# Kernel optimization log

Measured on AMD Instinct MI355X. Metric: run time of the kernel, lower is better.

Reference implementation:

```python
import jax, jax.numpy as jnp
import numpy as np

B, CQ, CKV, E = 8, 256, 256, 256
H, W = 64, 64
HP, WP = 32, 32


def setup_inputs() -> dict:
    key = jax.random.key(0)
    ks = jax.random.split(key, 6)
    C = jax.random.normal(ks[0], (B, CQ, H, W), dtype=jnp.float32)
    P = jax.random.normal(ks[1], (B, CKV, HP, WP), dtype=jnp.float32)
    # 1x1 conv weights, kaiming-ish scale; stored as [out_ch, in_ch]
    theta_w = jax.random.normal(ks[2], (E, CQ), dtype=jnp.float32) * (1.0 / np.sqrt(CQ))
    phi_w = jax.random.normal(ks[3], (E, CKV), dtype=jnp.float32) * (1.0 / np.sqrt(CKV))
    g_w = jax.random.normal(ks[4], (E, CKV), dtype=jnp.float32) * (1.0 / np.sqrt(CKV))
    out_w = jax.random.normal(ks[5], (CQ, E), dtype=jnp.float32) * (1.0 / np.sqrt(E))
    return {"C": C, "P": P, "theta_w": theta_w, "phi_w": phi_w, "g_w": g_w, "out_w": out_w}


def reference(C, P, theta_w, phi_w, g_w, out_w):
    b, _, h, w = C.shape
    e = theta_w.shape[0]
    # 1x1 convs are channel GEMMs
    theta_C = jnp.einsum('bchw,ec->behw', C, theta_w).reshape(b, e, h * w)   # [B,E,Nq]
    phi_P = jnp.einsum('bchw,ec->behw', P, phi_w).reshape(b, e, -1)          # [B,E,Nkv]
    g_P = jnp.einsum('bchw,ec->behw', P, g_w).reshape(b, e, -1)              # [B,E,Nkv]
    attn = jnp.einsum('ben,bem->bnm', theta_C, phi_P) / (e ** 0.5)           # [B,Nq,Nkv]
    attn = jax.nn.softmax(attn, axis=-1)
    out = jnp.einsum('bem,bnm->ben', g_P, attn).reshape(b, e, h, w)          # [B,E,H,W]
    out = jnp.einsum('behw,ce->bchw', out, out_w)                            # [B,CQ,H,W]
    return jnp.concatenate([C, out], axis=1)
```

## Files before the change

kernel.cpp:

```cpp
#include <hip/hip_runtime.h>


typedef __attribute__((ext_vector_type(8))) short short8;
typedef __attribute__((ext_vector_type(16))) float f32x16;
typedef unsigned short ushort_t;

__device__ __forceinline__ unsigned short f2bf(float f) {
    unsigned int u = __float_as_uint(f);
    u += 0x7FFFu + ((u >> 16) & 1u);
    return (unsigned short)(u >> 16);
}
__device__ __forceinline__ unsigned int pack2bf(float a, float b) {
    return (unsigned int)f2bf(a) | ((unsigned int)f2bf(b) << 16);
}
__device__ __forceinline__ void gload16(const ushort_t* g, ushort_t* l) {
    __builtin_amdgcn_global_load_lds(
        (const __attribute__((address_space(1))) unsigned int*)g,
        (__attribute__((address_space(3))) unsigned int*)l, 16, 0, 0);
}
__device__ __forceinline__ f32x16 zero16() {
    f32x16 z;
#pragma unroll
    for (int i = 0; i < 16; ++i) z[i] = 0.f;
    return z;
}

__global__ __launch_bounds__(256) void ct_cvt(const float* __restrict__ X,
                                              ushort_t* __restrict__ xT) {
    const int N = 4096;
    int b = blockIdx.z, c0 = blockIdx.y * 64, n0 = blockIdx.x * 64;
    int t = threadIdx.x;
    __shared__ float Xs[64][68];
    const float* Xb = X + ((size_t)b * 256 + c0) * N + n0;
    int cl = t >> 4, nl = (t & 15) * 4;
#pragma unroll
    for (int ci = 0; ci < 4; ++ci) {
        int c = ci * 16 + cl;
        float4 v = *(const float4*)(Xb + (size_t)c * N + nl);
        *(float4*)&Xs[c][nl] = v;
    }
    __syncthreads();
    ushort_t* xb = xT + (size_t)b * ((size_t)N * 256);
    int nl2 = t & 63, cgb = t >> 6;
#pragma unroll
    for (int cp = 0; cp < 2; ++cp) {
        int cg = cp * 4 + cgb;
        int cb = c0 + cg * 8;
        int n = n0 + nl2;
        short8 v;
#pragma unroll
        for (int u = 0; u < 8; ++u) v[u] = (short)f2bf(Xs[cg * 8 + u][nl2]);
        size_t i16 = ((size_t)(n >> 5) * 16 + (cb >> 4)) * 64 + ((cb >> 3) & 1) * 32 + (n & 31);
        *(short8*)(xb + i16 * 8) = v;
    }
}

__global__ __launch_bounds__(256) void prep_small(const float* __restrict__ P,
                                                  const float* __restrict__ thw,
                                                  const float* __restrict__ phw,
                                                  const float* __restrict__ ow,
                                                  const float* __restrict__ gw,
                                                  ushort_t* __restrict__ pT,
                                                  ushort_t* __restrict__ thc,
                                                  ushort_t* __restrict__ phc,
                                                  ushort_t* __restrict__ w2c) {
    int blk = blockIdx.x;
    int t = threadIdx.x;
    __shared__ float Xs[64][68];
    if (blk < 512) {
        const int N = 1024;
        int bx = blk & 15, by = (blk >> 4) & 3, b = blk >> 6;
        int n0 = bx * 64, c0 = by * 64;
        const float* Xb = P + ((size_t)b * 256 + c0) * N + n0;
        int cl = t >> 4, nl = (t & 15) * 4;
#pragma unroll
        for (int ci = 0; ci < 4; ++ci) {
            int c = ci * 16 + cl;
            *(float4*)&Xs[c][nl] = *(const float4*)(Xb + (size_t)c * N + nl);
        }
        __syncthreads();
        ushort_t* xb = pT + (size_t)b * ((size_t)N * 256);
        int nl2 = t & 63, cgb = t >> 6;
#pragma unroll
        for (int cp = 0; cp < 2; ++cp) {
            int cg = cp * 4 + cgb;
            int cb = c0 + cg * 8;
            int n = n0 + nl2;
            short8 v;
#pragma unroll
            for (int u = 0; u < 8; ++u) v[u] = (short)f2bf(Xs[cg * 8 + u][nl2]);
            size_t i16 = ((size_t)(n >> 5) * 16 + (cb >> 4)) * 64 + ((cb >> 3) & 1) * 32 + (n & 31);
            *(short8*)(xb + i16 * 8) = v;
        }
    } else if (blk < 1024) {
        int r = blk - 512;
        int which = r >> 8;
        int e = r & 255, c = t;
        const float* src = which ? phw : thw;
        ushort_t* dst = which ? phc : thc;
        int idx = ((((e >> 5) * 16 + (c >> 4)) * 64 + ((c >> 3) & 1) * 32 + (e & 31)) << 3) + (c & 7);
        dst[idx] = f2bf(src[e * 256 + c]);
    } else {
        int c0 = (blk - 1024) * 8;
        float acc[8] = {};
        for (int e = 0; e < 256; ++e) {
            float g = gw[e * 256 + t];
#pragma unroll
            for (int i = 0; i < 8; ++i) acc[i] += ow[(c0 + i) * 256 + e] * g;
        }
#pragma unroll
        for (int i = 0; i < 8; ++i) {
            int c = c0 + i, k = t;
            int idx = ((((c >> 5) * 16 + (k >> 4)) * 64 + ((k >> 3) & 1) * 32 + (c & 31)) << 3) + (k & 7);
            w2c[idx] = f2bf(acc[i]);
        }
    }
}

__global__ __launch_bounds__(256, 2) void proj_mfma(const ushort_t* __restrict__ thc,
                                                    const ushort_t* __restrict__ phc,
                                                    const ushort_t* __restrict__ w2c,
                                                    const ushort_t* __restrict__ cT,
                                                    const ushort_t* __restrict__ pT,
                                                    ushort_t* __restrict__ thetaA,
                                                    ushort_t* __restrict__ phiA,
                                                    ushort_t* __restrict__ gVx) {
    int blk = blockIdx.x;
    int tid = threadIdx.x, lane = tid & 63, wid = tid >> 6;
    int l31 = lane & 31, lh = lane >> 5;
    int role, b, nt;
    const ushort_t *Wc, *xTb;
    ushort_t* outp;
    float scale = 1.f;
    if (blk < 256) {
        role = 0; b = blk & 7; nt = blk >> 3;
        Wc = thc; xTb = cT + (size_t)b * 1048576; outp = thetaA + (size_t)b * 1048576;
        scale = 1.4426950408889634f / 16.0f;
    } else if (blk < 320) {
        int r = blk - 256; role = 1; b = r & 7; nt = r >> 3;
        Wc = phc; xTb = pT + (size_t)b * 262144; outp = phiA + (size_t)b * 262144;
    } else {
        int r = blk - 320; role = 2; b = r & 7; nt = r >> 3;
        Wc = w2c; xTb = pT + (size_t)b * 262144; outp = gVx + (size_t)b * 262144;
    }
    const int n0 = nt * 128 + wid * 32;
    const int ncr = (n0 >> 5) * 16;

    f32x16 o[8];
#pragma unroll
    for (int f = 0; f < 8; ++f) o[f] = zero16();

#pragma unroll
    for (int ks = 0; ks < 16; ++ks) {
        short8 xf = *(const short8*)(xTb + ((size_t)(ncr + ks) * 64 + lane) * 8);
#pragma unroll
        for (int f = 0; f < 8; ++f) {
            short8 wf = *(const short8*)(Wc + ((size_t)(f * 16 + ks) * 64 + lane) * 8);
            o[f] = __builtin_amdgcn_mfma_f32_32x32x16_bf16(wf, xf, o[f], 0, 0, 0);
        }
    }

    if (role < 2) {
#pragma unroll
        for (int f = 0; f < 8; ++f) {
#pragma unroll
            for (int rq = 0; rq < 4; ++rq) {
                uint2 st;
                st.x = pack2bf(o[f][4 * rq + 0] * scale, o[f][4 * rq + 1] * scale);
                st.y = pack2bf(o[f][4 * rq + 2] * scale, o[f][4 * rq + 3] * scale);
                size_t addr = ((size_t)(ncr + f * 2 + (rq >> 1)) * 64 + l31 + 32 * (rq & 1)) * 8 + 4 * lh;
                *(uint2*)(outp + addr) = st;
            }
        }
    } else {
        int kvq = (n0 >> 4) + (l31 >> 4);
        int lhw = 32 * ((l31 >> 3) & 1);
        int kl = l31 & 7;
#pragma unroll
        for (int f = 0; f < 8; ++f) {
#pragma unroll
            for (int r = 0; r < 16; ++r) {
                int crow = (r & 3) + 8 * (r >> 2) + 4 * lh;
                size_t addr = ((size_t)(f * 64 + kvq) * 64 + crow + lhw) * 8 + kl;
                outp[addr] = f2bf(o[f][r]);
            }
        }
    }
}

__global__ __launch_bounds__(512, 2) void attn7(const ushort_t* __restrict__ thetaA,
                                                const ushort_t* __restrict__ phiA,
                                                const ushort_t* __restrict__ gVx,
                                                const float* __restrict__ Cf,
                                                float* __restrict__ out) {
    const int b = blockIdx.x & 7, qt = blockIdx.x >> 3;
    const int tid = threadIdx.x, lane = tid & 63, wid = tid >> 6;
    const int l31 = lane & 31, lh = lane >> 5;
    const int h = wid >> 2, qg = wid & 3;

    __shared__ __align__(16) ushort_t smem[65536];
    __shared__ float rlS[4][32];

    const ushort_t* thA = thetaA + (size_t)b * 1048576;
    const ushort_t* phA = phiA + (size_t)b * 262144;
    const ushort_t* gVb = gVx + (size_t)b * 262144;

    auto stageK = [&](int j) {
        if ((wid & 2) == 0) {
            int hh = wid >> 2;
            const ushort_t* src = phA + (size_t)(2 * j + hh) * 8192 + (wid & 1) * 4096 + lane * 8;
            ushort_t* dst = smem + hh * 16384 + (j & 1) * 8192 + (wid & 1) * 4096;
#pragma unroll
            for (int i = 0; i < 8; ++i) gload16(src + i * 512, dst + i * 512);
        }
    };
    auto stageV = [&](int j) {
        if ((wid & 2) == 2) {
            int hh = wid >> 2;
#pragma unroll
            for (int cg2 = 0; cg2 < 4; ++cg2) {
                int cg = (wid & 1) * 4 + cg2;
#pragma unroll
                for (int jj = 0; jj < 2; ++jj) {
                    const ushort_t* src =
                        gVb + ((size_t)(cg * 64 + 4 * j + 2 * hh + jj) * 64 + lane) * 8;
                    ushort_t* dst = smem + 32768 + hh * 16384 + (j & 1) * 8192 + cg * 1024 + jj * 512;
                    gload16(src, dst);
                }
            }
        }
    };

    stageK(0); stageK(1); stageV(0);

    short8 qf[16];
    {
        const int qcr = (qt * 4 + qg) * 16;
#pragma unroll
        for (int ks = 0; ks < 16; ++ks)
            qf[ks] = *(const short8*)(thA + ((size_t)(qcr + ks) * 64 + lane) * 8);
    }

    f32x16 o[8];
#pragma unroll
    for (int f = 0; f < 8; ++f) o[f] = zero16();
    float rl = 0.f;

    const size_t cbase = (size_t)b * 1048576 + (size_t)qt * 128 + (size_t)l31 * 4;
    const size_t dofs = (size_t)b * 1048576;
    size_t cpo = 0;
    float4 cpv;

    asm volatile("s_waitcnt vmcnt(0)" ::: "memory");
    __builtin_amdgcn_s_barrier();
    __builtin_amdgcn_sched_barrier(0);

    f32x16 s = zero16();
    {
        const ushort_t* Kb = smem + h * 16384;
#pragma unroll
        for (int ks = 0; ks < 16; ++ks) {
            short8 kf = *(const short8*)(Kb + (size_t)ks * 512 + lane * 8);
            s = __builtin_amdgcn_mfma_f32_32x32x16_bf16(kf, qf[ks], s, 0, 0, 0);
        }
    }

    for (int it = 0; it < 16; ++it) {
        asm volatile("s_waitcnt vmcnt(0)" ::: "memory");
        __builtin_amdgcn_s_barrier();
        __builtin_amdgcn_sched_barrier(0);
        if (it < 14) stageK(it + 2);
        if (it < 15) stageV(it + 1);

        if (it > 0) *(float4*)(out + cpo + dofs) = cpv;
        cpo = cbase + (size_t)(it * 16 + 2 * wid + lh) * 4096;
        cpv = *(const float4*)(Cf + cpo);

        float ps = 0.f;
#pragma unroll
        for (int r = 0; r < 16; ++r) {
            s[r] = __builtin_amdgcn_exp2f(s[r]);
            ps += s[r];
        }
        ps += __shfl_xor(ps, 32);
        rl += ps;

        unsigned int a0 = pack2bf(s[0], s[1]),   b0 = pack2bf(s[4], s[5]);
        unsigned int a1 = pack2bf(s[2], s[3]),   b1 = pack2bf(s[6], s[7]);
        unsigned int a2 = pack2bf(s[8], s[9]),   b2 = pack2bf(s[12], s[13]);
        unsigned int a3 = pack2bf(s[10], s[11]), b3 = pack2bf(s[14], s[15]);
        asm volatile("v_permlane32_swap_b32 %0, %1" : "+v"(a0), "+v"(b0));
        asm volatile("v_permlane32_swap_b32 %0, %1" : "+v"(a1), "+v"(b1));
        asm volatile("v_permlane32_swap_b32 %0, %1" : "+v"(a2), "+v"(b2));
        asm volatile("v_permlane32_swap_b32 %0, %1" : "+v"(a3), "+v"(b3));
        union PW { unsigned int u[4]; short8 v; };
        PW p0; p0.u[0] = a0; p0.u[1] = a1; p0.u[2] = b0; p0.u[3] = b1;
        PW p1; p1.u[0] = a2; p1.u[1] = a3; p1.u[2] = b2; p1.u[3] = b3;

        const ushort_t* Vb = smem + 32768 + h * 16384 + (it & 1) * 8192;
        const ushort_t* Kb = smem + h * 16384 + ((it + 1) & 1) * 8192;
        __builtin_amdgcn_s_setprio(1);
        if (it < 15) {
            f32x16 sn = zero16();
#pragma unroll
            for (int ks2 = 0; ks2 < 2; ++ks2) {
                short8 pf = ks2 ? p1.v : p0.v;
#pragma unroll
                for (int f = 0; f < 8; ++f) {
                    short8 vf = *(const short8*)(Vb + (size_t)f * 1024 + ks2 * 512 + lane * 8);
                    o[f] = __builtin_amdgcn_mfma_f32_32x32x16_bf16(vf, pf, o[f], 0, 0, 0);
                    int ks = ks2 * 8 + f;
                    short8 kf = *(const short8*)(Kb + (size_t)ks * 512 + lane * 8);
                    sn = __builtin_amdgcn_mfma_f32_32x32x16_bf16(kf, qf[ks], sn, 0, 0, 0);
                }
            }
            s = sn;
        } else {
#pragma unroll
            for (int ks2 = 0; ks2 < 2; ++ks2) {
                short8 pf = ks2 ? p1.v : p0.v;
#pragma unroll
                for (int f = 0; f < 8; ++f) {
                    short8 vf = *(const short8*)(Vb + (size_t)f * 1024 + ks2 * 512 + lane * 8);
                    o[f] = __builtin_amdgcn_mfma_f32_32x32x16_bf16(vf, pf, o[f], 0, 0, 0);
                }
            }
        }
        __builtin_amdgcn_s_setprio(0);
        __builtin_amdgcn_sched_barrier(0);
    }

    *(float4*)(out + cpo + dofs) = cpv;

    __syncthreads();

    if (wid >= 4) {
        float* part = (float*)smem + (size_t)(wid - 4) * 8192;
#pragma unroll
        for (int f = 0; f < 8; ++f)
#pragma unroll
            for (int r = 0; r < 16; ++r) {
                int e = f * 32 + (r & 3) + 8 * (r >> 2) + 4 * lh;
                part[e * 32 + l31] = o[f][r];
            }
        if (lane < 32) rlS[wid - 4][l31] = rl;
    }
    __syncthreads();
    if (wid < 4) {
        float inv = 1.f / (rl + rlS[wid][l31]);
        const float* part = (const float*)smem + (size_t)wid * 8192;
        float* ob = out + (size_t)b * 2097152 + (size_t)256 * 4096 + qt * 128 + qg * 32 + l31;
#pragma unroll
        for (int f = 0; f < 8; ++f)
#pragma unroll
            for (int r = 0; r < 16; ++r) {
                int e = f * 32 + (r & 3) + 8 * (r >> 2) + 4 * lh;
                ob[(size_t)e * 4096] = (o[f][r] + part[e * 32 + l31]) * inv;
            }
    }
}


extern "C" void kernel_launch(void* const* d_in, const int* in_sizes, int n_in,
                              void* d_out, int out_size, void* d_ws, size_t ws_size,
                              hipStream_t stream) {
    const float* C       = (const float*)d_in[0];
    const float* P       = (const float*)d_in[1];
    const float* theta_w = (const float*)d_in[2];
    const float* phi_w   = (const float*)d_in[3];
    const float* g_w     = (const float*)d_in[4];
    const float* out_w   = (const float*)d_in[5];
    float* out = (float*)d_out;

    ushort_t* ws = (ushort_t*)d_ws;
    ushort_t* thetaA = ws;
    ushort_t* cT     = ws + 8388608;
    ushort_t* phiA   = ws + 16777216;
    ushort_t* pT     = ws + 18874368;
    ushort_t* gVx    = ws + 20971520;
    ushort_t* thWc   = ws + 23068672;
    ushort_t* phWc   = ws + 23134208;
    ushort_t* w2c    = ws + 23199744;

    prep_small<<<1056, 256, 0, stream>>>(P, theta_w, phi_w, out_w, g_w,
                                         pT, thWc, phWc, w2c);
    ct_cvt<<<dim3(64, 4, 8), 256, 0, stream>>>(C, cT);
    proj_mfma<<<384, 256, 0, stream>>>(thWc, phWc, w2c, cT, pT, thetaA, phiA, gVx);
    attn7<<<256, 512, 0, stream>>>(thetaA, phiA, gVx, C, out);
}
```

Measured before the change: 119.6 us.

## Fuse theta projection and C passthrough copy into attention kernel

Removes the separate C transpose/convert kernel and the theta projection blocks. The attention kernel now loads its 128-query tile of C into shared memory, writes the passthrough half of the output, and computes the scaled theta projection with MFMA directly into Q fragments using permlane swaps. This avoids writing and re-reading the bf16 cT and thetaA intermediates and drops one launch. In exchange, the attention kernel does extra work up front, uses more shared memory, and no longer overlaps the C copy with its main loop.

```diff
diff --git a/kernel.cpp b/kernel.cpp
--- a/kernel.cpp
+++ b/kernel.cpp
@@ -23,36 +23,6 @@
 #pragma unroll
     for (int i = 0; i < 16; ++i) z[i] = 0.f;
     return z;
-}
-
-__global__ __launch_bounds__(256) void ct_cvt(const float* __restrict__ X,
-                                              ushort_t* __restrict__ xT) {
-    const int N = 4096;
-    int b = blockIdx.z, c0 = blockIdx.y * 64, n0 = blockIdx.x * 64;
-    int t = threadIdx.x;
-    __shared__ float Xs[64][68];
-    const float* Xb = X + ((size_t)b * 256 + c0) * N + n0;
-    int cl = t >> 4, nl = (t & 15) * 4;
-#pragma unroll
-    for (int ci = 0; ci < 4; ++ci) {
-        int c = ci * 16 + cl;
-        float4 v = *(const float4*)(Xb + (size_t)c * N + nl);
-        *(float4*)&Xs[c][nl] = v;
-    }
-    __syncthreads();
-    ushort_t* xb = xT + (size_t)b * ((size_t)N * 256);
-    int nl2 = t & 63, cgb = t >> 6;
-#pragma unroll
-    for (int cp = 0; cp < 2; ++cp) {
-        int cg = cp * 4 + cgb;
-        int cb = c0 + cg * 8;
-        int n = n0 + nl2;
-        short8 v;
-#pragma unroll
-        for (int u = 0; u < 8; ++u) v[u] = (short)f2bf(Xs[cg * 8 + u][nl2]);
-        size_t i16 = ((size_t)(n >> 5) * 16 + (cb >> 4)) * 64 + ((cb >> 3) & 1) * 32 + (n & 31);
-        *(short8*)(xb + i16 * 8) = v;
-    }
 }
 
 __global__ __launch_bounds__(256) void prep_small(const float* __restrict__ P,
@@ -117,32 +87,19 @@
     }
 }
 
-__global__ __launch_bounds__(256, 2) void proj_mfma(const ushort_t* __restrict__ thc,
-                                                    const ushort_t* __restrict__ phc,
+__global__ __launch_bounds__(256, 2) void proj_mfma(const ushort_t* __restrict__ phc,
                                                     const ushort_t* __restrict__ w2c,
-                                                    const ushort_t* __restrict__ cT,
                                                     const ushort_t* __restrict__ pT,
-                                                    ushort_t* __restrict__ thetaA,
                                                     ushort_t* __restrict__ phiA,
                                                     ushort_t* __restrict__ gVx) {
     int blk = blockIdx.x;
     int tid = threadIdx.x, lane = tid & 63, wid = tid >> 6;
     int l31 = lane & 31, lh = lane >> 5;
-    int role, b, nt;
-    const ushort_t *Wc, *xTb;
-    ushort_t* outp;
-    float scale = 1.f;
-    if (blk < 256) {
-        role = 0; b = blk & 7; nt = blk >> 3;
-        Wc = thc; xTb = cT + (size_t)b * 1048576; outp = thetaA + (size_t)b * 1048576;
-        scale = 1.4426950408889634f / 16.0f;
-    } else if (blk < 320) {
-        int r = blk - 256; role = 1; b = r & 7; nt = r >> 3;
-        Wc = phc; xTb = pT + (size_t)b * 262144; outp = phiA + (size_t)b * 262144;
-    } else {
-        int r = blk - 320; role = 2; b = r & 7; nt = r >> 3;
-        Wc = w2c; xTb = pT + (size_t)b * 262144; outp = gVx + (size_t)b * 262144;
-    }
+    int role = blk >> 6;
+    int r = blk & 63, b = r & 7, nt = r >> 3;
+    const ushort_t* Wc = role ? w2c : phc;
+    const ushort_t* xTb = pT + (size_t)b * 262144;
+    ushort_t* outp = (role ? gVx : phiA) + (size_t)b * 262144;
     const int n0 = nt * 128 + wid * 32;
     const int ncr = (n0 >> 5) * 16;
 
@@ -160,14 +117,14 @@
         }
     }
 
-    if (role < 2) {
+    if (!role) {
 #pragma unroll
         for (int f = 0; f < 8; ++f) {
 #pragma unroll
             for (int rq = 0; rq < 4; ++rq) {
                 uint2 st;
-                st.x = pack2bf(o[f][4 * rq + 0] * scale, o[f][4 * rq + 1] * scale);
-                st.y = pack2bf(o[f][4 * rq + 2] * scale, o[f][4 * rq + 3] * scale);
+                st.x = pack2bf(o[f][4 * rq + 0], o[f][4 * rq + 1]);
+                st.y = pack2bf(o[f][4 * rq + 2], o[f][4 * rq + 3]);
                 size_t addr = ((size_t)(ncr + f * 2 + (rq >> 1)) * 64 + l31 + 32 * (rq & 1)) * 8 + 4 * lh;
                 *(uint2*)(outp + addr) = st;
             }
@@ -179,16 +136,16 @@
 #pragma unroll
         for (int f = 0; f < 8; ++f) {
 #pragma unroll
-            for (int r = 0; r < 16; ++r) {
-                int crow = (r & 3) + 8 * (r >> 2) + 4 * lh;
+            for (int r2 = 0; r2 < 16; ++r2) {
+                int crow = (r2 & 3) + 8 * (r2 >> 2) + 4 * lh;
                 size_t addr = ((size_t)(f * 64 + kvq) * 64 + crow + lhw) * 8 + kl;
-                outp[addr] = f2bf(o[f][r]);
-            }
-        }
-    }
-}
-
-__global__ __launch_bounds__(512, 2) void attn7(const ushort_t* __restrict__ thetaA,
+                outp[addr] = f2bf(o[f][r2]);
+            }
+        }
+    }
+}
+
+__global__ __launch_bounds__(512, 2) void attn8(const ushort_t* __restrict__ thc,
                                                 const ushort_t* __restrict__ phiA,
                                                 const ushort_t* __restrict__ gVx,
                                                 const float* __restrict__ Cf,
@@ -198,12 +155,72 @@
     const int l31 = lane & 31, lh = lane >> 5;
     const int h = wid >> 2, qg = wid & 3;
 
-    __shared__ __align__(16) ushort_t smem[65536];
+    __shared__ __align__(16) ushort_t smem[67584];
     __shared__ float rlS[4][32];
 
-    const ushort_t* thA = thetaA + (size_t)b * 1048576;
     const ushort_t* phA = phiA + (size_t)b * 262144;
     const ushort_t* gVb = gVx + (size_t)b * 262144;
+
+    {
+        float* Xf = (float*)smem;
+        const float* Cb = Cf + (size_t)b * 1048576 + (size_t)qt * 128;
+        float* outC = out + (size_t)b * 2097152 + (size_t)qt * 128;
+#pragma unroll
+        for (int i = 0; i < 16; ++i) {
+            int idx = i * 512 + tid;
+            int r = idx >> 5, c4 = (idx & 31) * 4;
+            float4 v = *(const float4*)(Cb + (size_t)r * 4096 + c4);
+            *(float4*)(outC + (size_t)r * 4096 + c4) = v;
+            *(float4*)(Xf + r * 132 + c4) = v;
+        }
+        __syncthreads();
+    }
+
+    f32x16 o[8];
+#pragma unroll
+    for (int f = 0; f < 8; ++f) o[f] = zero16();
+
+    {
+        const float* Xf = (const float*)smem;
+        const int q = qg * 32 + l31;
+#pragma unroll
+        for (int ks = 0; ks < 16; ++ks) {
+            const int cb = ks * 16 + lh * 8;
+            union PW { unsigned int u[4]; short8 v; } xw;
+#pragma unroll
+            for (int jj = 0; jj < 4; ++jj)
+                xw.u[jj] = pack2bf(Xf[(cb + 2 * jj) * 132 + q],
+                                   Xf[(cb + 2 * jj + 1) * 132 + q]);
+#pragma unroll
+            for (int f = 0; f < 8; ++f) {
+                short8 wf = *(const short8*)(thc + ((size_t)(f * 16 + ks) * 64 + lane) * 8);
+                o[f] = __builtin_amdgcn_mfma_f32_32x32x16_bf16(wf, xw.v, o[f], 0, 0, 0);
+            }
+        }
+    }
+
+    short8 qf[16];
+    {
+        const float TH = 1.4426950408889634f / 16.0f;
+#pragma unroll
+        for (int f = 0; f < 8; ++f) {
+#pragma unroll
+            for (int u = 0; u < 2; ++u) {
+                unsigned int A0 = pack2bf(o[f][8 * u + 0] * TH, o[f][8 * u + 1] * TH);
+                unsigned int A1 = pack2bf(o[f][8 * u + 2] * TH, o[f][8 * u + 3] * TH);
+                unsigned int B0 = pack2bf(o[f][8 * u + 4] * TH, o[f][8 * u + 5] * TH);
+                unsigned int B1 = pack2bf(o[f][8 * u + 6] * TH, o[f][8 * u + 7] * TH);
+                asm volatile("v_permlane32_swap_b32 %0, %1" : "+v"(A0), "+v"(B0));
+                asm volatile("v_permlane32_swap_b32 %0, %1" : "+v"(A1), "+v"(B1));
+                union PW { unsigned int u[4]; short8 v; } pw;
+                pw.u[0] = A0; pw.u[1] = A1; pw.u[2] = B0; pw.u[3] = B1;
+                qf[f * 2 + u] = pw.v;
+            }
+        }
+#pragma unroll
+        for (int f = 0; f < 8; ++f) o[f] = zero16();
+    }
+    __syncthreads();
 
     auto stageK = [&](int j) {
         if ((wid & 2) == 0) {
@@ -233,23 +250,7 @@
 
     stageK(0); stageK(1); stageV(0);
 
-    short8 qf[16];
-    {
-        const int qcr = (qt * 4 + qg) * 16;
-#pragma unroll
-        for (int ks = 0; ks < 16; ++ks)
-            qf[ks] = *(const short8*)(thA + ((size_t)(qcr + ks) * 64 + lane) * 8);
-    }
-
-    f32x16 o[8];
-#pragma unroll
-    for (int f = 0; f < 8; ++f) o[f] = zero16();
     float rl = 0.f;
-
-    const size_t cbase = (size_t)b * 1048576 + (size_t)qt * 128 + (size_t)l31 * 4;
-    const size_t dofs = (size_t)b * 1048576;
-    size_t cpo = 0;
-    float4 cpv;
 
     asm volatile("s_waitcnt vmcnt(0)" ::: "memory");
     __builtin_amdgcn_s_barrier();
@@ -271,10 +272,6 @@
         __builtin_amdgcn_sched_barrier(0);
         if (it < 14) stageK(it + 2);
         if (it < 15) stageV(it + 1);
-
-        if (it > 0) *(float4*)(out + cpo + dofs) = cpv;
-        cpo = cbase + (size_t)(it * 16 + 2 * wid + lh) * 4096;
-        cpv = *(const float4*)(Cf + cpo);
 
         float ps = 0.f;
 #pragma unroll
@@ -330,8 +327,6 @@
         __builtin_amdgcn_sched_barrier(0);
     }
 
-    *(float4*)(out + cpo + dofs) = cpv;
-
     __syncthreads();
 
     if (wid >= 4) {
@@ -373,18 +368,15 @@
     float* out = (float*)d_out;
 
     ushort_t* ws = (ushort_t*)d_ws;
-    ushort_t* thetaA = ws;
-    ushort_t* cT     = ws + 8388608;
-    ushort_t* phiA   = ws + 16777216;
-    ushort_t* pT     = ws + 18874368;
-    ushort_t* gVx    = ws + 20971520;
-    ushort_t* thWc   = ws + 23068672;
-    ushort_t* phWc   = ws + 23134208;
-    ushort_t* w2c    = ws + 23199744;
+    ushort_t* phiA = ws;
+    ushort_t* pT   = ws + 2097152;
+    ushort_t* gVx  = ws + 4194304;
+    ushort_t* thWc = ws + 6291456;
+    ushort_t* phWc = ws + 6356992;
+    ushort_t* w2c  = ws + 6422528;
 
     prep_small<<<1056, 256, 0, stream>>>(P, theta_w, phi_w, out_w, g_w,
                                          pT, thWc, phWc, w2c);
-    ct_cvt<<<dim3(64, 4, 8), 256, 0, stream>>>(C, cT);
-    proj_mfma<<<384, 256, 0, stream>>>(thWc, phWc, w2c, cT, pT, thetaA, phiA, gVx);
-    attn7<<<256, 512, 0, stream>>>(thetaA, phiA, gVx, C, out);
-}
+    proj_mfma<<<128, 256, 0, stream>>>(phWc, w2c, pT, phiA, gVx);
+    attn8<<<256, 512, 0, stream>>>(thWc, phiA, gVx, C, out);
+}
```

New measurement: 123.2 us. 3.0% more time.
